# Kernel optimization log

Measured on AMD Instinct MI355X. Metric: run time of the kernel, lower is better.

The kernel has to match this reference:

```python
import jax, jax.numpy as jnp
import numpy as np

B, R, N, E, DIN, DOUT = 2, 2, 50000, 500000, 128, 128


def setup_inputs() -> dict:
    key = jax.random.key(0)
    k_x, k_src, k_dst, k_val, k_w = jax.random.split(key, 5)
    x = jax.random.normal(k_x, (B, N, DIN), dtype=jnp.float32)
    edge_src = jax.random.randint(k_src, (B, R, E), 0, N, dtype=jnp.int32)
    edge_dst = jax.random.randint(k_dst, (B, R, E), 0, N, dtype=jnp.int32)
    edge_val = jax.random.uniform(k_val, (B, R, E), dtype=jnp.float32)
    # Glorot-uniform init as in init_weight: range = sqrt(6/(fan_in+fan_out))
    init_range = float(np.sqrt(6.0 / (DIN + DOUT)))
    weights = jax.random.uniform(k_w, (R, DIN, DOUT), minval=-init_range,
                                 maxval=init_range, dtype=jnp.float32)
    bias = jnp.zeros((DOUT,), dtype=jnp.float32)
    return {"x": x, "edge_val": edge_val, "weights": weights, "bias": bias,
            "edge_src": edge_src, "edge_dst": edge_dst}


def reference(x, edge_val, weights, bias, edge_src, edge_dst):
    # Dense feature transform per relation: pre_sup = x @ W_r  -> [B, R, N, DOUT]
    pre = jnp.einsum('bnd,rde->brne', x, weights)
    bi = jnp.arange(B)[:, None, None]   # [B,1,1]
    ri = jnp.arange(R)[None, :, None]   # [1,R,1]
    # Sparse adjacency matmul A_r @ pre_sup:
    # out[dst] += A[dst, src] * pre_sup[src]  (edge list form)
    msgs = edge_val[..., None] * pre[bi, ri, edge_src]          # [B,R,E,DOUT]
    agg = jnp.zeros((B, R, N, DOUT), dtype=pre.dtype)
    agg = agg.at[bi, ri, edge_dst].add(msgs)                    # scatter-add
    # Sum across relations (tf.add_n), add bias, relu activation
    out = agg.sum(axis=1) + bias                                # [B,N,DOUT]
    return jax.nn.relu(out)
```

## Files before the change

kernel.cpp:

```cpp
#include <hip/hip_runtime.h>

#define BB 2
#define RR 2
#define NN 50000
#define EE 500000
#define DD 128
#define NSLOT 4
#define BSH 6
#define BSZ 64
#define NB 782
#define FT 8192
#define FBLK 62
#define SCAP 2048
#define DSTR 50048

#define A_PRE  0u
#define A_REC  12800000u
#define A_CNT  20800000u
#define A_OFS  20812544u
#define A_CUR  20825088u
#define A_DOF  20837632u
#define A_WT   21638400u

#define B_PRE  0u
#define B_REC  25600000u
#define B_CNT  33600000u
#define B_OFS  33612544u
#define B_CUR  33625088u
#define B_DOF  33637632u
#define B_WT   34438400u
#define B_TOTAL 34503936u

typedef __attribute__((ext_vector_type(8))) short bf16x8;
typedef __attribute__((ext_vector_type(4))) float f32x4;

__device__ __forceinline__ unsigned short f2bf(float f) {
    unsigned int u = __float_as_uint(f);
    u += 0x7fffu + ((u >> 16) & 1u);
    return (unsigned short)(u >> 16);
}

__device__ __forceinline__ bf16x8 pack8(float4 a, float4 b) {
    bf16x8 r;
    r[0] = (short)f2bf(a.x); r[1] = (short)f2bf(a.y);
    r[2] = (short)f2bf(a.z); r[3] = (short)f2bf(a.w);
    r[4] = (short)f2bf(b.x); r[5] = (short)f2bf(b.y);
    r[6] = (short)f2bf(b.z); r[7] = (short)f2bf(b.w);
    return r;
}

__global__ __launch_bounds__(256) void wprep_kernel(
    const float* __restrict__ w, unsigned short* __restrict__ wt)
{
    int idx = blockIdx.x * 256 + threadIdx.x;
    if (idx >= RR * DD * DD) return;
    int r = idx >> 14;
    int k = (idx >> 7) & (DD - 1);
    int n = idx & (DD - 1);
    wt[((size_t)r * DD + n) * DD + k] = f2bf(w[idx]);
}

template <int RST>
__global__ __launch_bounds__(256) void gemm_mfma_kernel(
    const float* __restrict__ x,
    const unsigned short* __restrict__ wt,
    unsigned short* __restrict__ pre)
{
    const int tid = threadIdx.x;
    const int w = tid >> 6, lane = tid & 63;
    const int wr = w >> 1, wc = w & 1;
    const int lq = lane >> 4, lr = lane & 15;
    const int row0 = blockIdx.x * 128;

    f32x4 acc[4][4] = {};

    #pragma unroll
    for (int ks = 0; ks < 4; ++ks) {
        const int k0 = ks * 32 + lq * 8;
        bf16x8 a[4], b[4];
        #pragma unroll
        for (int mi = 0; mi < 4; ++mi) {
            int row = row0 + wr * 64 + mi * 16 + lr;
            float4 v0 = make_float4(0.f, 0.f, 0.f, 0.f);
            float4 v1 = make_float4(0.f, 0.f, 0.f, 0.f);
            if (row < NN) {
                const float* p = x + (size_t)row * DD + k0;
                v0 = *(const float4*)p;
                v1 = *(const float4*)(p + 4);
            }
            a[mi] = pack8(v0, v1);
        }
        #pragma unroll
        for (int ni = 0; ni < 4; ++ni) {
            int n = wc * 64 + ni * 16 + lr;
            b[ni] = *(const bf16x8*)(wt + (size_t)n * DD + k0);
        }
        #pragma unroll
        for (int mi = 0; mi < 4; ++mi)
            #pragma unroll
            for (int ni = 0; ni < 4; ++ni)
                acc[mi][ni] = __builtin_amdgcn_mfma_f32_16x16x32_bf16(
                    a[mi], b[ni], acc[mi][ni], 0, 0, 0);
    }

    #pragma unroll
    for (int mi = 0; mi < 4; ++mi) {
        #pragma unroll
        for (int q = 0; q < 4; ++q) {
            int row = row0 + wr * 64 + mi * 16 + lq * 4 + q;
            if (row < NN) {
                #pragma unroll
                for (int ni = 0; ni < 4; ++ni) {
                    int col = wc * 64 + ni * 16 + lr;
                    pre[(size_t)row * RST + col] = f2bf(acc[mi][ni][q]);
                }
            }
        }
    }
}

__global__ __launch_bounds__(256) void hist_kernel(
    const int* __restrict__ edst, int* __restrict__ counts)
{
    __shared__ int h[NB];
    for (int i = threadIdx.x; i < NB; i += 256) h[i] = 0;
    __syncthreads();
    const int slot = blockIdx.y;
    const int* ed = edst + (size_t)slot * EE;
    for (int e = blockIdx.x * 256 + threadIdx.x; e < EE; e += 128 * 256)
        atomicAdd(&h[ed[e] >> BSH], 1);
    __syncthreads();
    int* c = counts + slot * NB;
    for (int i = threadIdx.x; i < NB; i += 256) {
        int v = h[i];
        if (v) atomicAdd(&c[i], v);
    }
}

__global__ __launch_bounds__(1024) void scan_kernel(
    const int* __restrict__ counts, int* __restrict__ offsets,
    int* __restrict__ cursor)
{
    __shared__ int s[1024];
    const int slot = blockIdx.x;
    int v = (threadIdx.x < NB) ? counts[slot * NB + threadIdx.x] : 0;
    s[threadIdx.x] = v;
    for (int o = 1; o < 1024; o <<= 1) {
        __syncthreads();
        int t = (threadIdx.x >= o) ? s[threadIdx.x - o] : 0;
        __syncthreads();
        s[threadIdx.x] += t;
    }
    __syncthreads();
    if (threadIdx.x < NB) {
        int incl = s[threadIdx.x];
        offsets[slot * 784 + threadIdx.x + 1] = incl;
        cursor[slot * NB + threadIdx.x] = incl - v;
    }
    if (threadIdx.x == 0) offsets[slot * 784] = 0;
}

__global__ __launch_bounds__(1024) void fill_kernel(
    const int* __restrict__ esrc, const int* __restrict__ edst,
    const float* __restrict__ ev, int* __restrict__ cursor,
    unsigned int* __restrict__ recs)
{
    __shared__ int lh[NB];
    __shared__ int lbase[NB];
    const int slot = blockIdx.y;
    const size_t eb = (size_t)slot * EE;
    const int e0 = blockIdx.x * FT;

    for (int i = threadIdx.x; i < NB; i += 1024) lh[i] = 0;
    __syncthreads();
    for (int t = 0; t < FT; t += 1024) {
        int e = e0 + t + threadIdx.x;
        if (e < EE) atomicAdd(&lh[edst[eb + e] >> BSH], 1);
    }
    __syncthreads();
    for (int i = threadIdx.x; i < NB; i += 1024) {
        int c = lh[i];
        lbase[i] = c ? atomicAdd(&cursor[slot * NB + i], c) : 0;
        lh[i] = 0;
    }
    __syncthreads();
    for (int t = 0; t < FT; t += 1024) {
        int e = e0 + t + threadIdx.x;
        if (e < EE) {
            int d = edst[eb + e];
            int bk = d >> BSH;
            unsigned vq = (unsigned)__builtin_rintf(ev[eb + e] * 1023.0f);
            unsigned rec = (unsigned)esrc[eb + e] |
                           ((unsigned)(d & (BSZ - 1)) << 16) | (vq << 22);
            int p = lbase[bk] + atomicAdd(&lh[bk], 1);
            recs[eb + p] = rec;
        }
    }
}

__global__ __launch_bounds__(256) void sort_kernel(
    unsigned int* __restrict__ recs, const int* __restrict__ offsets,
    int* __restrict__ dofs)
{
    __shared__ unsigned int lrec[SCAP];
    __shared__ int cnt[BSZ];
    __shared__ int cur[BSZ];
    const int bk = blockIdx.x, slot = blockIdx.y;
    unsigned int* rp = recs + (size_t)slot * EE;
    const int s = offsets[slot * 784 + bk], e = offsets[slot * 784 + bk + 1];
    const int n = e - s;

    for (int i = threadIdx.x; i < n; i += 256) lrec[i] = rp[s + i];
    if (threadIdx.x < BSZ) cnt[threadIdx.x] = 0;
    __syncthreads();
    for (int i = threadIdx.x; i < n; i += 256)
        atomicAdd(&cnt[(lrec[i] >> 16) & (BSZ - 1)], 1);
    __syncthreads();
    if (threadIdx.x < 64) {
        int v = cnt[threadIdx.x];
        int incl = v;
        #pragma unroll
        for (int o = 1; o < 64; o <<= 1) {
            int t = __shfl_up(incl, o, 64);
            if (threadIdx.x >= o) incl += t;
        }
        int excl = incl - v;
        cur[threadIdx.x] = excl;
        dofs[(size_t)slot * DSTR + bk * BSZ + threadIdx.x] = s + excl;
    }
    __syncthreads();
    for (int i = threadIdx.x; i < n; i += 256) {
        unsigned r = lrec[i];
        int p = atomicAdd(&cur[(r >> 16) & (BSZ - 1)], 1);
        rp[s + p] = r;
    }
}

#define DEQ (1.0f / 1023.0f)
#define LO16(u) __uint_as_float((u) << 16)
#define HI16(u) __uint_as_float((u) & 0xffff0000u)

template <int STRIDE, int OFF>
__device__ __forceinline__ void gacc(const unsigned short* __restrict__ pre,
                                     const unsigned int* __restrict__ rp,
                                     int i, int e, int lane2,
                                     float& acc0, float& acc1)
{
    for (; i + 8 <= e; i += 8) {
        unsigned q[8], u[8];
        #pragma unroll
        for (int j = 0; j < 8; ++j) q[j] = rp[i + j];
        #pragma unroll
        for (int j = 0; j < 8; ++j)
            u[j] = *(const unsigned*)(pre + (size_t)(q[j] & 0xffffu) * STRIDE + OFF + lane2);
        #pragma unroll
        for (int j = 0; j < 8; ++j) {
            float s = (float)(q[j] >> 22) * DEQ;
            acc0 = fmaf(s, LO16(u[j]), acc0);
            acc1 = fmaf(s, HI16(u[j]), acc1);
        }
    }
    if (i + 4 <= e) {
        unsigned q[4], u[4];
        #pragma unroll
        for (int j = 0; j < 4; ++j) q[j] = rp[i + j];
        #pragma unroll
        for (int j = 0; j < 4; ++j)
            u[j] = *(const unsigned*)(pre + (size_t)(q[j] & 0xffffu) * STRIDE + OFF + lane2);
        #pragma unroll
        for (int j = 0; j < 4; ++j) {
            float s = (float)(q[j] >> 22) * DEQ;
            acc0 = fmaf(s, LO16(u[j]), acc0);
            acc1 = fmaf(s, HI16(u[j]), acc1);
        }
        i += 4;
    }
    if (i + 2 <= e) {
        unsigned q0 = rp[i], q1 = rp[i + 1];
        unsigned u0 = *(const unsigned*)(pre + (size_t)(q0 & 0xffffu) * STRIDE + OFF + lane2);
        unsigned u1 = *(const unsigned*)(pre + (size_t)(q1 & 0xffffu) * STRIDE + OFF + lane2);
        float s0 = (float)(q0 >> 22) * DEQ, s1 = (float)(q1 >> 22) * DEQ;
        acc0 = fmaf(s0, LO16(u0), acc0); acc1 = fmaf(s0, HI16(u0), acc1);
        acc0 = fmaf(s1, LO16(u1), acc0); acc1 = fmaf(s1, HI16(u1), acc1);
        i += 2;
    }
    if (i < e) {
        unsigned q0 = rp[i];
        unsigned u0 = *(const unsigned*)(pre + (size_t)(q0 & 0xffffu) * STRIDE + OFF + lane2);
        float s0 = (float)(q0 >> 22) * DEQ;
        acc0 = fmaf(s0, LO16(u0), acc0); acc1 = fmaf(s0, HI16(u0), acc1);
    }
}

template <int FINAL>
__global__ __launch_bounds__(256) void gather_kernel(
    const unsigned short* __restrict__ pre, const unsigned int* __restrict__ rp,
    const int* __restrict__ dofs, const float* __restrict__ bias,
    float* __restrict__ out)
{
    const int d = blockIdx.x * 4 + (threadIdx.x >> 6);
    const int lane = threadIdx.x & 63;
    const int lane2 = lane * 2;
    const int i = dofs[d], e = dofs[d + 1];

    float2* o = (float2*)(out + (size_t)d * DD + lane2);
    float2 pv;
    float b0, b1;
    if (FINAL) {
        pv = *o;
        b0 = bias[lane2]; b1 = bias[lane2 + 1];
    }

    float acc0 = 0.f, acc1 = 0.f;
    gacc<DD, 0>(pre, rp, i, e, lane2, acc0, acc1);

    if (FINAL) {
        pv.x = fmaxf(pv.x + acc0 + b0, 0.f);
        pv.y = fmaxf(pv.y + acc1 + b1, 0.f);
        *o = pv;
    } else {
        *o = make_float2(acc0, acc1);
    }
}

__global__ __launch_bounds__(256) void gather_dual_kernel(
    const unsigned short* __restrict__ preb,
    const unsigned int* __restrict__ rp0, const unsigned int* __restrict__ rp1,
    const int* __restrict__ dofs0, const int* __restrict__ dofs1,
    const float* __restrict__ bias, float* __restrict__ out)
{
    const int d = blockIdx.x * 4 + (threadIdx.x >> 6);
    const int lane = threadIdx.x & 63;
    const int lane2 = lane * 2;
    const int i0 = dofs0[d], e0 = dofs0[d + 1];
    const int i1 = dofs1[d], e1 = dofs1[d + 1];

    float acc0 = 0.f, acc1 = 0.f;
    gacc<2 * DD, 0>(preb, rp0, i0, e0, lane2, acc0, acc1);
    gacc<2 * DD, DD>(preb, rp1, i1, e1, lane2, acc0, acc1);

    float2 pv;
    pv.x = fmaxf(acc0 + bias[lane2], 0.f);
    pv.y = fmaxf(acc1 + bias[lane2 + 1], 0.f);
    *(float2*)(out + (size_t)d * DD + lane2) = pv;
}

extern "C" void kernel_launch(void* const* d_in, const int* in_sizes, int n_in,
                              void* d_out, int out_size, void* d_ws, size_t ws_size,
                              hipStream_t stream) {
    const float* x     = (const float*)d_in[0];
    const float* eval_ = (const float*)d_in[1];
    const float* w     = (const float*)d_in[2];
    const float* bias  = (const float*)d_in[3];
    const int*   esrc  = (const int*)d_in[4];
    const int*   edst  = (const int*)d_in[5];
    float* out = (float*)d_out;

    const bool useB = (ws_size >= (size_t)B_TOTAL);

    char* ws = (char*)d_ws;
    unsigned short* pre     = (unsigned short*)(ws + (useB ? B_PRE : A_PRE));
    unsigned int*   recs    = (unsigned int*)(ws + (useB ? B_REC : A_REC));
    int*            counts  = (int*)(ws + (useB ? B_CNT : A_CNT));
    int*            offsets = (int*)(ws + (useB ? B_OFS : A_OFS));
    int*            cursor  = (int*)(ws + (useB ? B_CUR : A_CUR));
    int*            dofs    = (int*)(ws + (useB ? B_DOF : A_DOF));
    unsigned short* wt      = (unsigned short*)(ws + (useB ? B_WT : A_WT));

    const dim3 blk(256);

    hipMemsetAsync(counts, 0, NSLOT * NB * sizeof(int), stream);
    wprep_kernel<<<(RR * DD * DD + 255) / 256, blk, 0, stream>>>(w, wt);

    hist_kernel<<<dim3(128, NSLOT), blk, 0, stream>>>(edst, counts);
    scan_kernel<<<dim3(NSLOT), dim3(1024), 0, stream>>>(counts, offsets, cursor);
    fill_kernel<<<dim3(FBLK, NSLOT), dim3(1024), 0, stream>>>(
        esrc, edst, eval_, cursor, recs);
    sort_kernel<<<dim3(NB, NSLOT), blk, 0, stream>>>(recs, offsets, dofs);

    const dim3 gemm_grid((NN + 127) / 128);
    const dim3 gath_grid(NN / 4);

    if (useB) {
        for (int b = 0; b < BB; ++b) {
            const int s0 = b * RR, s1 = b * RR + 1;
            gemm_mfma_kernel<2 * DD><<<gemm_grid, blk, 0, stream>>>(
                x + (size_t)b * NN * DD, wt, pre);
            gemm_mfma_kernel<2 * DD><<<gemm_grid, blk, 0, stream>>>(
                x + (size_t)b * NN * DD, wt + (size_t)DD * DD, pre + DD);
            gather_dual_kernel<<<gath_grid, blk, 0, stream>>>(
                pre, recs + (size_t)s0 * EE, recs + (size_t)s1 * EE,
                dofs + (size_t)s0 * DSTR, dofs + (size_t)s1 * DSTR,
                bias, out + (size_t)b * NN * DD);
        }
    } else {
        for (int b = 0; b < BB; ++b) {
            for (int r = 0; r < RR; ++r) {
                const int slot = b * RR + r;
                gemm_mfma_kernel<DD><<<gemm_grid, blk, 0, stream>>>(
                    x + (size_t)b * NN * DD, wt + (size_t)r * DD * DD, pre);
                if (r == 0)
                    gather_kernel<0><<<gath_grid, blk, 0, stream>>>(
                        pre, recs + (size_t)slot * EE, dofs + (size_t)slot * DSTR,
                        bias, out + (size_t)b * NN * DD);
                else
                    gather_kernel<1><<<gath_grid, blk, 0, stream>>>(
                        pre, recs + (size_t)slot * EE, dofs + (size_t)slot * DSTR,
                        bias, out + (size_t)b * NN * DD);
            }
        }
    }
}
```

Measured before the change: 196.5 us.

## Fuse both relation GEMMs into one 512-thread kernel and use 32-bit gather addressing

```diff
diff --git a/kernel.cpp b/kernel.cpp
--- a/kernel.cpp
+++ b/kernel.cpp
@@ -119,6 +119,64 @@
     }
 }
 
+__global__ __launch_bounds__(512) void gemm_mfma_dual_kernel(
+    const float* __restrict__ x,
+    const unsigned short* __restrict__ wt,
+    unsigned short* __restrict__ pre)
+{
+    const int tid = threadIdx.x;
+    const int w = tid >> 6, lane = tid & 63;
+    const int wr = w >> 2, wc = w & 3;
+    const int lq = lane >> 4, lr = lane & 15;
+    const int row0 = blockIdx.x * 128;
+
+    f32x4 acc[4][4] = {};
+
+    #pragma unroll
+    for (int ks = 0; ks < 4; ++ks) {
+        const int k0 = ks * 32 + lq * 8;
+        bf16x8 a[4], b[4];
+        #pragma unroll
+        for (int mi = 0; mi < 4; ++mi) {
+            int row = row0 + wr * 64 + mi * 16 + lr;
+            float4 v0 = make_float4(0.f, 0.f, 0.f, 0.f);
+            float4 v1 = make_float4(0.f, 0.f, 0.f, 0.f);
+            if (row < NN) {
+                const float* p = x + (size_t)row * DD + k0;
+                v0 = *(const float4*)p;
+                v1 = *(const float4*)(p + 4);
+            }
+            a[mi] = pack8(v0, v1);
+        }
+        #pragma unroll
+        for (int ni = 0; ni < 4; ++ni) {
+            int n = wc * 64 + ni * 16 + lr;
+            b[ni] = *(const bf16x8*)(wt + (size_t)n * DD + k0);
+        }
+        #pragma unroll
+        for (int mi = 0; mi < 4; ++mi)
+            #pragma unroll
+            for (int ni = 0; ni < 4; ++ni)
+                acc[mi][ni] = __builtin_amdgcn_mfma_f32_16x16x32_bf16(
+                    a[mi], b[ni], acc[mi][ni], 0, 0, 0);
+    }
+
+    #pragma unroll
+    for (int mi = 0; mi < 4; ++mi) {
+        #pragma unroll
+        for (int q = 0; q < 4; ++q) {
+            int row = row0 + wr * 64 + mi * 16 + lq * 4 + q;
+            if (row < NN) {
+                #pragma unroll
+                for (int ni = 0; ni < 4; ++ni) {
+                    int col = wc * 64 + ni * 16 + lr;
+                    pre[(size_t)row * (2 * DD) + col] = f2bf(acc[mi][ni][q]);
+                }
+            }
+        }
+    }
+}
+
 __global__ __launch_bounds__(256) void hist_kernel(
     const int* __restrict__ edst, int* __restrict__ counts)
 {
@@ -240,19 +298,20 @@
 #define LO16(u) __uint_as_float((u) << 16)
 #define HI16(u) __uint_as_float((u) & 0xffff0000u)
 
-template <int STRIDE, int OFF>
+template <int SH, int OFF>
 __device__ __forceinline__ void gacc(const unsigned short* __restrict__ pre,
                                      const unsigned int* __restrict__ rp,
-                                     int i, int e, int lane2,
+                                     unsigned i, unsigned e, unsigned lane2,
                                      float& acc0, float& acc1)
 {
+    const unsigned base = (unsigned)OFF + lane2;
     for (; i + 8 <= e; i += 8) {
         unsigned q[8], u[8];
         #pragma unroll
         for (int j = 0; j < 8; ++j) q[j] = rp[i + j];
         #pragma unroll
         for (int j = 0; j < 8; ++j)
-            u[j] = *(const unsigned*)(pre + (size_t)(q[j] & 0xffffu) * STRIDE + OFF + lane2);
+            u[j] = *(const unsigned*)(pre + (((q[j] & 0xffffu) << SH) + base));
         #pragma unroll
         for (int j = 0; j < 8; ++j) {
             float s = (float)(q[j] >> 22) * DEQ;
@@ -266,7 +325,7 @@
         for (int j = 0; j < 4; ++j) q[j] = rp[i + j];
         #pragma unroll
         for (int j = 0; j < 4; ++j)
-            u[j] = *(const unsigned*)(pre + (size_t)(q[j] & 0xffffu) * STRIDE + OFF + lane2);
+            u[j] = *(const unsigned*)(pre + (((q[j] & 0xffffu) << SH) + base));
         #pragma unroll
         for (int j = 0; j < 4; ++j) {
             float s = (float)(q[j] >> 22) * DEQ;
@@ -277,8 +336,8 @@
     }
     if (i + 2 <= e) {
         unsigned q0 = rp[i], q1 = rp[i + 1];
-        unsigned u0 = *(const unsigned*)(pre + (size_t)(q0 & 0xffffu) * STRIDE + OFF + lane2);
-        unsigned u1 = *(const unsigned*)(pre + (size_t)(q1 & 0xffffu) * STRIDE + OFF + lane2);
+        unsigned u0 = *(const unsigned*)(pre + (((q0 & 0xffffu) << SH) + base));
+        unsigned u1 = *(const unsigned*)(pre + (((q1 & 0xffffu) << SH) + base));
         float s0 = (float)(q0 >> 22) * DEQ, s1 = (float)(q1 >> 22) * DEQ;
         acc0 = fmaf(s0, LO16(u0), acc0); acc1 = fmaf(s0, HI16(u0), acc1);
         acc0 = fmaf(s1, LO16(u1), acc0); acc1 = fmaf(s1, HI16(u1), acc1);
@@ -286,7 +345,7 @@
     }
     if (i < e) {
         unsigned q0 = rp[i];
-        unsigned u0 = *(const unsigned*)(pre + (size_t)(q0 & 0xffffu) * STRIDE + OFF + lane2);
+        unsigned u0 = *(const unsigned*)(pre + (((q0 & 0xffffu) << SH) + base));
         float s0 = (float)(q0 >> 22) * DEQ;
         acc0 = fmaf(s0, LO16(u0), acc0); acc1 = fmaf(s0, HI16(u0), acc1);
     }
@@ -299,9 +358,8 @@
     float* __restrict__ out)
 {
     const int d = blockIdx.x * 4 + (threadIdx.x >> 6);
-    const int lane = threadIdx.x & 63;
-    const int lane2 = lane * 2;
-    const int i = dofs[d], e = dofs[d + 1];
+    const unsigned lane2 = (threadIdx.x & 63) * 2;
+    const unsigned i = dofs[d], e = dofs[d + 1];
 
     float2* o = (float2*)(out + (size_t)d * DD + lane2);
     float2 pv;
@@ -312,7 +370,7 @@
     }
 
     float acc0 = 0.f, acc1 = 0.f;
-    gacc<DD, 0>(pre, rp, i, e, lane2, acc0, acc1);
+    gacc<7, 0>(pre, rp, i, e, lane2, acc0, acc1);
 
     if (FINAL) {
         pv.x = fmaxf(pv.x + acc0 + b0, 0.f);
@@ -330,14 +388,13 @@
     const float* __restrict__ bias, float* __restrict__ out)
 {
     const int d = blockIdx.x * 4 + (threadIdx.x >> 6);
-    const int lane = threadIdx.x & 63;
-    const int lane2 = lane * 2;
-    const int i0 = dofs0[d], e0 = dofs0[d + 1];
-    const int i1 = dofs1[d], e1 = dofs1[d + 1];
+    const unsigned lane2 = (threadIdx.x & 63) * 2;
+    const unsigned i0 = dofs0[d], e0 = dofs0[d + 1];
+    const unsigned i1 = dofs1[d], e1 = dofs1[d + 1];
 
     float acc0 = 0.f, acc1 = 0.f;
-    gacc<2 * DD, 0>(preb, rp0, i0, e0, lane2, acc0, acc1);
-    gacc<2 * DD, DD>(preb, rp1, i1, e1, lane2, acc0, acc1);
+    gacc<8, 0>(preb, rp0, i0, e0, lane2, acc0, acc1);
+    gacc<8, DD>(preb, rp1, i1, e1, lane2, acc0, acc1);
 
     float2 pv;
     pv.x = fmaxf(acc0 + bias[lane2], 0.f);
@@ -384,10 +441,8 @@
     if (useB) {
         for (int b = 0; b < BB; ++b) {
             const int s0 = b * RR, s1 = b * RR + 1;
-            gemm_mfma_kernel<2 * DD><<<gemm_grid, blk, 0, stream>>>(
+            gemm_mfma_dual_kernel<<<gemm_grid, dim3(512), 0, stream>>>(
                 x + (size_t)b * NN * DD, wt, pre);
-            gemm_mfma_kernel<2 * DD><<<gemm_grid, blk, 0, stream>>>(
-                x + (size_t)b * NN * DD, wt + (size_t)DD * DD, pre + DD);
             gather_dual_kernel<<<gath_grid, blk, 0, stream>>>(
                 pre, recs + (size_t)s0 * EE, recs + (size_t)s1 * EE,
                 dofs + (size_t)s0 * DSTR, dofs + (size_t)s1 * DSTR,
```

Result: faster. 191.4 us (-2.6%).

## Reorder to aggregate-then-transform with one concatenated-relation GEMM per batch

Applied to the files above, without the earlier changes.

```diff
diff --git a/kernel.cpp b/kernel.cpp
--- a/kernel.cpp
+++ b/kernel.cpp
@@ -14,22 +14,13 @@
 #define SCAP 2048
 #define DSTR 50048
 
-#define A_PRE  0u
-#define A_REC  12800000u
-#define A_CNT  20800000u
-#define A_OFS  20812544u
-#define A_CUR  20825088u
-#define A_DOF  20837632u
-#define A_WT   21638400u
-
-#define B_PRE  0u
-#define B_REC  25600000u
-#define B_CNT  33600000u
-#define B_OFS  33612544u
-#define B_CUR  33625088u
-#define B_DOF  33637632u
-#define B_WT   34438400u
-#define B_TOTAL 34503936u
+#define XB_OFF  0u
+#define REC_OFF 12800000u
+#define CNT_OFF 20800000u
+#define OFS_OFF 20812544u
+#define CUR_OFF 20825088u
+#define DOF_OFF 20837632u
+#define WT_OFF  21638400u
 
 typedef __attribute__((ext_vector_type(8))) short bf16x8;
 typedef __attribute__((ext_vector_type(4))) float f32x4;
@@ -50,73 +41,24 @@
 }
 
 __global__ __launch_bounds__(256) void wprep_kernel(
-    const float* __restrict__ w, unsigned short* __restrict__ wt)
+    const float* __restrict__ w, unsigned short* __restrict__ wt2)
 {
     int idx = blockIdx.x * 256 + threadIdx.x;
     if (idx >= RR * DD * DD) return;
     int r = idx >> 14;
     int k = (idx >> 7) & (DD - 1);
     int n = idx & (DD - 1);
-    wt[((size_t)r * DD + n) * DD + k] = f2bf(w[idx]);
-}
-
-template <int RST>
-__global__ __launch_bounds__(256) void gemm_mfma_kernel(
-    const float* __restrict__ x,
-    const unsigned short* __restrict__ wt,
-    unsigned short* __restrict__ pre)
-{
-    const int tid = threadIdx.x;
-    const int w = tid >> 6, lane = tid & 63;
-    const int wr = w >> 1, wc = w & 1;
-    const int lq = lane >> 4, lr = lane & 15;
-    const int row0 = blockIdx.x * 128;
-
-    f32x4 acc[4][4] = {};
-
-    #pragma unroll
-    for (int ks = 0; ks < 4; ++ks) {
-        const int k0 = ks * 32 + lq * 8;
-        bf16x8 a[4], b[4];
-        #pragma unroll
-        for (int mi = 0; mi < 4; ++mi) {
-            int row = row0 + wr * 64 + mi * 16 + lr;
-            float4 v0 = make_float4(0.f, 0.f, 0.f, 0.f);
-            float4 v1 = make_float4(0.f, 0.f, 0.f, 0.f);
-            if (row < NN) {
-                const float* p = x + (size_t)row * DD + k0;
-                v0 = *(const float4*)p;
-                v1 = *(const float4*)(p + 4);
-            }
-            a[mi] = pack8(v0, v1);
-        }
-        #pragma unroll
-        for (int ni = 0; ni < 4; ++ni) {
-            int n = wc * 64 + ni * 16 + lr;
-            b[ni] = *(const bf16x8*)(wt + (size_t)n * DD + k0);
-        }
-        #pragma unroll
-        for (int mi = 0; mi < 4; ++mi)
-            #pragma unroll
-            for (int ni = 0; ni < 4; ++ni)
-                acc[mi][ni] = __builtin_amdgcn_mfma_f32_16x16x32_bf16(
-                    a[mi], b[ni], acc[mi][ni], 0, 0, 0);
-    }
-
-    #pragma unroll
-    for (int mi = 0; mi < 4; ++mi) {
-        #pragma unroll
-        for (int q = 0; q < 4; ++q) {
-            int row = row0 + wr * 64 + mi * 16 + lq * 4 + q;
-            if (row < NN) {
-                #pragma unroll
-                for (int ni = 0; ni < 4; ++ni) {
-                    int col = wc * 64 + ni * 16 + lr;
-                    pre[(size_t)row * RST + col] = f2bf(acc[mi][ni][q]);
-                }
-            }
-        }
-    }
+    wt2[(size_t)n * 256 + r * DD + k] = f2bf(w[idx]);
+}
+
+__global__ __launch_bounds__(256) void cast_kernel(
+    const float* __restrict__ x, unsigned short* __restrict__ xb)
+{
+    int i8 = (blockIdx.x * 256 + threadIdx.x) * 8;
+    if (i8 >= NN * DD) return;
+    float4 v0 = *(const float4*)&x[i8];
+    float4 v1 = *(const float4*)&x[i8 + 4];
+    *(bf16x8*)&xb[i8] = pack8(v0, v1);
 }
 
 __global__ __launch_bounds__(256) void hist_kernel(
@@ -240,10 +182,9 @@
 #define LO16(u) __uint_as_float((u) << 16)
 #define HI16(u) __uint_as_float((u) & 0xffff0000u)
 
-template <int STRIDE, int OFF>
-__device__ __forceinline__ void gacc(const unsigned short* __restrict__ pre,
+__device__ __forceinline__ void gacc(const unsigned short* __restrict__ xb,
                                      const unsigned int* __restrict__ rp,
-                                     int i, int e, int lane2,
+                                     unsigned i, unsigned e, unsigned lane2,
                                      float& acc0, float& acc1)
 {
     for (; i + 8 <= e; i += 8) {
@@ -252,7 +193,7 @@
         for (int j = 0; j < 8; ++j) q[j] = rp[i + j];
         #pragma unroll
         for (int j = 0; j < 8; ++j)
-            u[j] = *(const unsigned*)(pre + (size_t)(q[j] & 0xffffu) * STRIDE + OFF + lane2);
+            u[j] = *(const unsigned*)(xb + (((q[j] & 0xffffu) << 7) + lane2));
         #pragma unroll
         for (int j = 0; j < 8; ++j) {
             float s = (float)(q[j] >> 22) * DEQ;
@@ -266,7 +207,7 @@
         for (int j = 0; j < 4; ++j) q[j] = rp[i + j];
         #pragma unroll
         for (int j = 0; j < 4; ++j)
-            u[j] = *(const unsigned*)(pre + (size_t)(q[j] & 0xffffu) * STRIDE + OFF + lane2);
+            u[j] = *(const unsigned*)(xb + (((q[j] & 0xffffu) << 7) + lane2));
         #pragma unroll
         for (int j = 0; j < 4; ++j) {
             float s = (float)(q[j] >> 22) * DEQ;
@@ -275,74 +216,89 @@
         }
         i += 4;
     }
-    if (i + 2 <= e) {
-        unsigned q0 = rp[i], q1 = rp[i + 1];
-        unsigned u0 = *(const unsigned*)(pre + (size_t)(q0 & 0xffffu) * STRIDE + OFF + lane2);
-        unsigned u1 = *(const unsigned*)(pre + (size_t)(q1 & 0xffffu) * STRIDE + OFF + lane2);
-        float s0 = (float)(q0 >> 22) * DEQ, s1 = (float)(q1 >> 22) * DEQ;
-        acc0 = fmaf(s0, LO16(u0), acc0); acc1 = fmaf(s0, HI16(u0), acc1);
-        acc0 = fmaf(s1, LO16(u1), acc0); acc1 = fmaf(s1, HI16(u1), acc1);
-        i += 2;
-    }
-    if (i < e) {
+    for (; i < e; ++i) {
         unsigned q0 = rp[i];
-        unsigned u0 = *(const unsigned*)(pre + (size_t)(q0 & 0xffffu) * STRIDE + OFF + lane2);
+        unsigned u0 = *(const unsigned*)(xb + (((q0 & 0xffffu) << 7) + lane2));
         float s0 = (float)(q0 >> 22) * DEQ;
         acc0 = fmaf(s0, LO16(u0), acc0); acc1 = fmaf(s0, HI16(u0), acc1);
     }
 }
 
-template <int FINAL>
-__global__ __launch_bounds__(256) void gather_kernel(
-    const unsigned short* __restrict__ pre, const unsigned int* __restrict__ rp,
-    const int* __restrict__ dofs, const float* __restrict__ bias,
-    float* __restrict__ out)
-{
-    const int d = blockIdx.x * 4 + (threadIdx.x >> 6);
-    const int lane = threadIdx.x & 63;
-    const int lane2 = lane * 2;
-    const int i = dofs[d], e = dofs[d + 1];
-
-    float2* o = (float2*)(out + (size_t)d * DD + lane2);
-    float2 pv;
-    float b0, b1;
-    if (FINAL) {
-        pv = *o;
-        b0 = bias[lane2]; b1 = bias[lane2 + 1];
-    }
-
-    float acc0 = 0.f, acc1 = 0.f;
-    gacc<DD, 0>(pre, rp, i, e, lane2, acc0, acc1);
-
-    if (FINAL) {
-        pv.x = fmaxf(pv.x + acc0 + b0, 0.f);
-        pv.y = fmaxf(pv.y + acc1 + b1, 0.f);
-        *o = pv;
-    } else {
-        *o = make_float2(acc0, acc1);
-    }
-}
-
 __global__ __launch_bounds__(256) void gather_dual_kernel(
-    const unsigned short* __restrict__ preb,
+    const unsigned short* __restrict__ xb,
     const unsigned int* __restrict__ rp0, const unsigned int* __restrict__ rp1,
     const int* __restrict__ dofs0, const int* __restrict__ dofs1,
-    const float* __restrict__ bias, float* __restrict__ out)
+    unsigned short* __restrict__ agg)
 {
     const int d = blockIdx.x * 4 + (threadIdx.x >> 6);
-    const int lane = threadIdx.x & 63;
-    const int lane2 = lane * 2;
-    const int i0 = dofs0[d], e0 = dofs0[d + 1];
-    const int i1 = dofs1[d], e1 = dofs1[d + 1];
-
-    float acc0 = 0.f, acc1 = 0.f;
-    gacc<2 * DD, 0>(preb, rp0, i0, e0, lane2, acc0, acc1);
-    gacc<2 * DD, DD>(preb, rp1, i1, e1, lane2, acc0, acc1);
-
-    float2 pv;
-    pv.x = fmaxf(acc0 + bias[lane2], 0.f);
-    pv.y = fmaxf(acc1 + bias[lane2 + 1], 0.f);
-    *(float2*)(out + (size_t)d * DD + lane2) = pv;
+    const unsigned lane2 = (threadIdx.x & 63) * 2;
+
+    float a0 = 0.f, a1 = 0.f, b0 = 0.f, b1 = 0.f;
+    gacc(xb, rp0, dofs0[d], dofs0[d + 1], lane2, a0, a1);
+    gacc(xb, rp1, dofs1[d], dofs1[d + 1], lane2, b0, b1);
+
+    unsigned short* row = agg + (size_t)d * 256;
+    unsigned p0 = (unsigned)f2bf(a0) | ((unsigned)f2bf(a1) << 16);
+    unsigned p1 = (unsigned)f2bf(b0) | ((unsigned)f2bf(b1) << 16);
+    *(unsigned*)(row + lane2) = p0;
+    *(unsigned*)(row + DD + lane2) = p1;
+}
+
+__global__ __launch_bounds__(256) void gemm_agg_kernel(
+    const unsigned short* __restrict__ wt2,
+    const float* __restrict__ bias,
+    float* __restrict__ outb)
+{
+    const unsigned short* agg = (const unsigned short*)outb;
+    const int tid = threadIdx.x;
+    const int w = tid >> 6, lane = tid & 63;
+    const int wr = w >> 1, wc = w & 1;
+    const int lq = lane >> 4, lr = lane & 15;
+    const int row0 = blockIdx.x * 128;
+
+    f32x4 acc[4][4] = {};
+
+    #pragma unroll
+    for (int ks = 0; ks < 8; ++ks) {
+        const int k0 = ks * 32 + lq * 8;
+        bf16x8 a[4], b[4];
+        #pragma unroll
+        for (int mi = 0; mi < 4; ++mi) {
+            int row = row0 + wr * 64 + mi * 16 + lr;
+            bf16x8 v = {};
+            if (row < NN) v = *(const bf16x8*)(agg + (size_t)row * 256 + k0);
+            a[mi] = v;
+        }
+        #pragma unroll
+        for (int ni = 0; ni < 4; ++ni) {
+            int n = wc * 64 + ni * 16 + lr;
+            b[ni] = *(const bf16x8*)(wt2 + (size_t)n * 256 + k0);
+        }
+        #pragma unroll
+        for (int mi = 0; mi < 4; ++mi)
+            #pragma unroll
+            for (int ni = 0; ni < 4; ++ni)
+                acc[mi][ni] = __builtin_amdgcn_mfma_f32_16x16x32_bf16(
+                    a[mi], b[ni], acc[mi][ni], 0, 0, 0);
+    }
+
+    __syncthreads();
+
+    #pragma unroll
+    for (int mi = 0; mi < 4; ++mi) {
+        #pragma unroll
+        for (int q = 0; q < 4; ++q) {
+            int row = row0 + wr * 64 + mi * 16 + lq * 4 + q;
+            if (row < NN) {
+                #pragma unroll
+                for (int ni = 0; ni < 4; ++ni) {
+                    int col = wc * 64 + ni * 16 + lr;
+                    outb[(size_t)row * DD + col] =
+                        fmaxf(acc[mi][ni][q] + bias[col], 0.f);
+                }
+            }
+        }
+    }
 }
 
 extern "C" void kernel_launch(void* const* d_in, const int* in_sizes, int n_in,
@@ -356,21 +312,19 @@
     const int*   edst  = (const int*)d_in[5];
     float* out = (float*)d_out;
 
-    const bool useB = (ws_size >= (size_t)B_TOTAL);
-
     char* ws = (char*)d_ws;
-    unsigned short* pre     = (unsigned short*)(ws + (useB ? B_PRE : A_PRE));
-    unsigned int*   recs    = (unsigned int*)(ws + (useB ? B_REC : A_REC));
-    int*            counts  = (int*)(ws + (useB ? B_CNT : A_CNT));
-    int*            offsets = (int*)(ws + (useB ? B_OFS : A_OFS));
-    int*            cursor  = (int*)(ws + (useB ? B_CUR : A_CUR));
-    int*            dofs    = (int*)(ws + (useB ? B_DOF : A_DOF));
-    unsigned short* wt      = (unsigned short*)(ws + (useB ? B_WT : A_WT));
+    unsigned short* xb      = (unsigned short*)(ws + XB_OFF);
+    unsigned int*   recs    = (unsigned int*)(ws + REC_OFF);
+    int*            counts  = (int*)(ws + CNT_OFF);
+    int*            offsets = (int*)(ws + OFS_OFF);
+    int*            cursor  = (int*)(ws + CUR_OFF);
+    int*            dofs    = (int*)(ws + DOF_OFF);
+    unsigned short* wt2     = (unsigned short*)(ws + WT_OFF);
 
     const dim3 blk(256);
 
     hipMemsetAsync(counts, 0, NSLOT * NB * sizeof(int), stream);
-    wprep_kernel<<<(RR * DD * DD + 255) / 256, blk, 0, stream>>>(w, wt);
+    wprep_kernel<<<(RR * DD * DD + 255) / 256, blk, 0, stream>>>(w, wt2);
 
     hist_kernel<<<dim3(128, NSLOT), blk, 0, stream>>>(edst, counts);
     scan_kernel<<<dim3(NSLOT), dim3(1024), 0, stream>>>(counts, offsets, cursor);
@@ -378,36 +332,18 @@
         esrc, edst, eval_, cursor, recs);
     sort_kernel<<<dim3(NB, NSLOT), blk, 0, stream>>>(recs, offsets, dofs);
 
+    const dim3 cast_grid((NN * DD / 8 + 255) / 256);
+    const dim3 gath_grid(NN / 4);
     const dim3 gemm_grid((NN + 127) / 128);
-    const dim3 gath_grid(NN / 4);
-
-    if (useB) {
-        for (int b = 0; b < BB; ++b) {
-            const int s0 = b * RR, s1 = b * RR + 1;
-            gemm_mfma_kernel<2 * DD><<<gemm_grid, blk, 0, stream>>>(
-                x + (size_t)b * NN * DD, wt, pre);
-            gemm_mfma_kernel<2 * DD><<<gemm_grid, blk, 0, stream>>>(
-                x + (size_t)b * NN * DD, wt + (size_t)DD * DD, pre + DD);
-            gather_dual_kernel<<<gath_grid, blk, 0, stream>>>(
-                pre, recs + (size_t)s0 * EE, recs + (size_t)s1 * EE,
-                dofs + (size_t)s0 * DSTR, dofs + (size_t)s1 * DSTR,
-                bias, out + (size_t)b * NN * DD);
-        }
-    } else {
-        for (int b = 0; b < BB; ++b) {
-            for (int r = 0; r < RR; ++r) {
-                const int slot = b * RR + r;
-                gemm_mfma_kernel<DD><<<gemm_grid, blk, 0, stream>>>(
-                    x + (size_t)b * NN * DD, wt + (size_t)r * DD * DD, pre);
-                if (r == 0)
-                    gather_kernel<0><<<gath_grid, blk, 0, stream>>>(
-                        pre, recs + (size_t)slot * EE, dofs + (size_t)slot * DSTR,
-                        bias, out + (size_t)b * NN * DD);
-                else
-                    gather_kernel<1><<<gath_grid, blk, 0, stream>>>(
-                        pre, recs + (size_t)slot * EE, dofs + (size_t)slot * DSTR,
-                        bias, out + (size_t)b * NN * DD);
-            }
-        }
-    }
-}
+
+    for (int b = 0; b < BB; ++b) {
+        const int s0 = b * RR, s1 = b * RR + 1;
+        float* outb = out + (size_t)b * NN * DD;
+        cast_kernel<<<cast_grid, blk, 0, stream>>>(x + (size_t)b * NN * DD, xb);
+        gather_dual_kernel<<<gath_grid, blk, 0, stream>>>(
+            xb, recs + (size_t)s0 * EE, recs + (size_t)s1 * EE,
+            dofs + (size_t)s0 * DSTR, dofs + (size_t)s1 * DSTR,
+            (unsigned short*)outb);
+        gemm_agg_kernel<<<gemm_grid, blk, 0, stream>>>(wt2, bias, outb);
+    }
+}
```

Result: faster. 191.2 us (-2.7%).
